# Kernel tuning notes

Measured on AMD Instinct MI355X. Metric: run time of the kernel, lower is better.

The kernel has to match this reference:

```python
import jax, jax.numpy as jnp
import numpy as np

B, C, H, W = 8, 192, 128, 128
NUM_HEADS = 4
EPS = 1e-12  # torch F.normalize default eps
DN = ('NCHW', 'OIHW', 'NCHW')


def setup_inputs() -> dict:
    key = jax.random.key(0)
    k1, k2, k3, k4 = jax.random.split(key, 4)
    x = jax.random.normal(k1, (B, C, H, W), dtype=jnp.float32)
    qkv_w = jax.random.normal(k2, (3 * C, C, 1, 1), dtype=jnp.float32) * 0.05
    dw_w = jax.random.normal(k3, (3 * C, 1, 3, 3), dtype=jnp.float32) * 0.1
    proj_w = jax.random.normal(k4, (C, C, 1, 1), dtype=jnp.float32) * 0.05
    temperature = jnp.ones((NUM_HEADS, 1, 1), dtype=jnp.float32)
    return {"x": x, "qkv_w": qkv_w, "dw_w": dw_w, "proj_w": proj_w,
            "temperature": temperature}


def _l2norm(t):
    # F.normalize(t, dim=-1): divide by max(||t||, eps)
    n = jnp.sqrt(jnp.sum(t * t, axis=-1, keepdims=True))
    return t / jnp.maximum(n, EPS)


def reference(x, qkv_w, dw_w, proj_w, temperature):
    b, c, h, w = x.shape
    nh = NUM_HEADS
    cph = c // nh
    # 1x1 conv -> depthwise 3x3 conv (groups = 3*dim)
    qkv = jax.lax.conv_general_dilated(x, qkv_w, (1, 1), 'VALID',
                                       dimension_numbers=DN)
    qkv = jax.lax.conv_general_dilated(qkv, dw_w, (1, 1), [(1, 1), (1, 1)],
                                       dimension_numbers=DN,
                                       feature_group_count=3 * c)
    q, k, v = jnp.split(qkv, 3, axis=1)
    # [b, nh, cph, h*w]
    q = q.reshape(b, nh, cph, h * w)
    k = k.reshape(b, nh, cph, h * w)
    v = v.reshape(b, nh, cph, h * w)
    q = _l2norm(q)
    k = _l2norm(k)
    # channel attention: [b, nh, cph, cph]
    attn = jnp.einsum('bhcn,bhdn->bhcd', q, k) * temperature
    attn = jax.nn.softmax(attn, axis=-1)
    out = jnp.einsum('bhcd,bhdn->bhcn', attn, v)
    out = out.reshape(b, c, h, w)
    return jax.lax.conv_general_dilated(out, proj_w, (1, 1), 'VALID',
                                        dimension_numbers=DN)
```

## Files before the change

### kernel.cpp

```cpp
#include <hip/hip_runtime.h>
#include <hip/hip_bf16.h>

typedef __hip_bfloat16 bf16;
typedef __attribute__((ext_vector_type(8))) __bf16 bf16x8;
typedef __attribute__((ext_vector_type(4))) float f32x4;

#define HW 16384

static __device__ __forceinline__ float b2f(bf16 v) { return __bfloat162float(v); }
static __device__ __forceinline__ bf16 f2b(float v) { return __float2bfloat16(v); }
static __device__ __forceinline__ float blo(unsigned int w) {
    return __uint_as_float(w << 16);
}
static __device__ __forceinline__ float bhi(unsigned int w) {
    return __uint_as_float(w & 0xffff0000u);
}
static __device__ __forceinline__ unsigned short f2bu(float v) {
    union { bf16 b; unsigned short u; } c; c.b = f2b(v); return c.u;
}
static __device__ __forceinline__ void stf(float* p, float v) { *p = v; }
static __device__ __forceinline__ void stf(bf16* p, float v)  { *p = f2b(v); }

static __device__ __forceinline__ void load8(const float* p, float* v) {
    const float4* q = (const float4*)p;
    float4 a = q[0], b = q[1];
    v[0] = a.x; v[1] = a.y; v[2] = a.z; v[3] = a.w;
    v[4] = b.x; v[5] = b.y; v[6] = b.z; v[7] = b.w;
}
static __device__ __forceinline__ void load8(const bf16* p, float* v) {
    uint4 u = *(const uint4*)p;
    v[0] = blo(u.x); v[1] = bhi(u.x); v[2] = blo(u.y); v[3] = bhi(u.y);
    v[4] = blo(u.z); v[5] = bhi(u.z); v[6] = blo(u.w); v[7] = bhi(u.w);
}

__global__ __launch_bounds__(256) void transpose_cast(
    const float* __restrict__ x, bf16* __restrict__ xT)
{
    __shared__ float T[64][65];
    const int k0 = blockIdx.x * 64, n0 = blockIdx.y * 64, b = blockIdx.z;
    const float* xb = x + ((size_t)(b * 192 + k0) << 14) + n0;

    for (int s = threadIdx.x; s < 64 * 16; s += 256) {
        int k = s >> 4, n4 = (s & 15) * 4;
        float4 v = *(const float4*)(xb + ((size_t)k << 14) + n4);
        T[k][n4] = v.x; T[k][n4 + 1] = v.y; T[k][n4 + 2] = v.z; T[k][n4 + 3] = v.w;
    }
    __syncthreads();

    bf16* xo = xT + ((size_t)b << 14) * 192 + (size_t)n0 * 192 + k0;
    for (int s = threadIdx.x; s < 64 * 8; s += 256) {
        int n = s >> 3, k8 = (s & 7) * 8;
        union { unsigned short u[8]; uint4 v; } o;
#pragma unroll
        for (int j = 0; j < 8; j++) o.u[j] = f2bu(T[k8 + j][n]);
        *(uint4*)(xo + (size_t)n * 192 + k8) = o.v;
    }
}

template <typename TY>
__global__ __launch_bounds__(256) void gemm_nk(
    const float* __restrict__ Wm, const bf16* __restrict__ Bt,
    TY* __restrict__ Y, int M, int N)
{
    const int mb = blockIdx.x, nb = blockIdx.y, b = blockIdx.z;
    const int m0 = mb * 64, n0 = nb * 128;
    TY* Yb = Y + (size_t)b * M * N;
    const bf16* Bb = Bt + ((size_t)b * N + n0) * 192;

    __shared__ __bf16 As[64][200];
    __shared__ __bf16 Bs[128][200];

    const int tid = threadIdx.x;
    for (int s = tid; s < 64 * 24; s += 256) {
        int m = s / 24, kq = (s % 24) * 8;
        float v[8];
        load8(Wm + (size_t)(m0 + m) * 192 + kq, v);
        bf16x8 pk;
#pragma unroll
        for (int j = 0; j < 8; j++) pk[j] = (__bf16)v[j];
        *(bf16x8*)&As[m][kq] = pk;
    }
    for (int s = tid; s < 128 * 24; s += 256) {
        int n = s / 24, kq = s % 24;
        *(uint4*)&Bs[n][kq * 8] = *(const uint4*)(Bb + (size_t)n * 192 + kq * 8);
    }
    __syncthreads();

    const int lane = tid & 63, wave = tid >> 6;
    const int wm = (wave & 1) * 32, wn = (wave >> 1) * 64;
    const int r16 = lane & 15, quad = lane >> 4;

    f32x4 acc[2][4];
#pragma unroll
    for (int i = 0; i < 2; i++)
#pragma unroll
        for (int f = 0; f < 4; f++) acc[i][f] = (f32x4){0.f, 0.f, 0.f, 0.f};

#pragma unroll
    for (int kc = 0; kc < 6; kc++) {
        const int kb = kc * 32 + quad * 8;
        bf16x8 a0 = *(const bf16x8*)&As[wm + r16][kb];
        bf16x8 a1 = *(const bf16x8*)&As[wm + 16 + r16][kb];
        bf16x8 b0 = *(const bf16x8*)&Bs[wn + r16][kb];
        bf16x8 b1 = *(const bf16x8*)&Bs[wn + 16 + r16][kb];
        bf16x8 b2 = *(const bf16x8*)&Bs[wn + 32 + r16][kb];
        bf16x8 b3 = *(const bf16x8*)&Bs[wn + 48 + r16][kb];
        acc[0][0] = __builtin_amdgcn_mfma_f32_16x16x32_bf16(a0, b0, acc[0][0], 0, 0, 0);
        acc[0][1] = __builtin_amdgcn_mfma_f32_16x16x32_bf16(a0, b1, acc[0][1], 0, 0, 0);
        acc[0][2] = __builtin_amdgcn_mfma_f32_16x16x32_bf16(a0, b2, acc[0][2], 0, 0, 0);
        acc[0][3] = __builtin_amdgcn_mfma_f32_16x16x32_bf16(a0, b3, acc[0][3], 0, 0, 0);
        acc[1][0] = __builtin_amdgcn_mfma_f32_16x16x32_bf16(a1, b0, acc[1][0], 0, 0, 0);
        acc[1][1] = __builtin_amdgcn_mfma_f32_16x16x32_bf16(a1, b1, acc[1][1], 0, 0, 0);
        acc[1][2] = __builtin_amdgcn_mfma_f32_16x16x32_bf16(a1, b2, acc[1][2], 0, 0, 0);
        acc[1][3] = __builtin_amdgcn_mfma_f32_16x16x32_bf16(a1, b3, acc[1][3], 0, 0, 0);
    }

#pragma unroll
    for (int i = 0; i < 2; i++)
#pragma unroll
        for (int f = 0; f < 4; f++) {
            int gr = m0 + wm + i * 16 + quad * 4;
            int gc = n0 + wn + f * 16 + r16;
#pragma unroll
            for (int r = 0; r < 4; r++)
                stf(Yb + (size_t)(gr + r) * N + gc, acc[i][f][r]);
        }
}

__global__ __launch_bounds__(256) void dwconv3x3(
    const bf16* __restrict__ in, const float* __restrict__ wdw,
    bf16* __restrict__ out)
{
    const int plane = blockIdx.x >> 2;
    const int ybase = (blockIdx.x & 3) << 5;
    const int c = plane % 576;
    const bf16* ip = in + ((size_t)plane << 14);

    __shared__ unsigned short Ls[34][128];

    for (int i = threadIdx.x; i < 34 * 16; i += 256) {
        int r = i >> 4, cx = i & 15;
        int y = ybase - 1 + r;
        uint4 v = make_uint4(0u, 0u, 0u, 0u);
        if (y >= 0 && y < 128) v = ((const uint4*)(ip + ((size_t)y << 7)))[cx];
        ((uint4*)Ls[r])[cx] = v;
    }

    float w[9];
#pragma unroll
    for (int i = 0; i < 9; i++) w[i] = wdw[c * 9 + i];

    __syncthreads();

    const int lr = threadIdx.x >> 3;
    const int c0 = (threadIdx.x & 7) << 4;

    float row[3][18];
#pragma unroll
    for (int r3 = 0; r3 < 3; r3++) {
        int rr = lr + r3;
        row[r3][0]  = c0 ? __uint_as_float((unsigned int)Ls[rr][c0 - 1] << 16) : 0.f;
        row[r3][17] = (c0 + 16 < 128) ? __uint_as_float((unsigned int)Ls[rr][c0 + 16] << 16) : 0.f;
        const uint4* rp = (const uint4*)&Ls[rr][c0];
        uint4 p0 = rp[0], p1 = rp[1];
        row[r3][1] = blo(p0.x); row[r3][2] = bhi(p0.x);
        row[r3][3] = blo(p0.y); row[r3][4] = bhi(p0.y);
        row[r3][5] = blo(p0.z); row[r3][6] = bhi(p0.z);
        row[r3][7] = blo(p0.w); row[r3][8] = bhi(p0.w);
        row[r3][9]  = blo(p1.x); row[r3][10] = bhi(p1.x);
        row[r3][11] = blo(p1.y); row[r3][12] = bhi(p1.y);
        row[r3][13] = blo(p1.z); row[r3][14] = bhi(p1.z);
        row[r3][15] = blo(p1.w); row[r3][16] = bhi(p1.w);
    }

    union { unsigned short s[16]; uint4 v[2]; } o;
#pragma unroll
    for (int j = 0; j < 16; j++) {
        float s = 0.f;
#pragma unroll
        for (int r3 = 0; r3 < 3; r3++)
            s += w[r3 * 3 + 0] * row[r3][j] + w[r3 * 3 + 1] * row[r3][j + 1]
               + w[r3 * 3 + 2] * row[r3][j + 2];
        o.s[j] = f2bu(s);
    }
    uint4* op = (uint4*)(out + ((size_t)plane << 14) + ((size_t)(ybase + lr) << 7) + c0);
    op[0] = o.v[0];
    op[1] = o.v[1];
}

__global__ __launch_bounds__(256) void rownorm(
    const bf16* __restrict__ qkv, float* __restrict__ rn)
{
    int r = blockIdx.x;
    int which = (r >= 1536) ? 1 : 0;
    int rr = r - which * 1536;
    int b = rr / 192, c = rr % 192;
    const bf16* p = qkv + ((size_t)(b * 576 + which * 192 + c) << 14);

    float s = 0.f;
    for (int i = threadIdx.x * 8; i < HW; i += 256 * 8) {
        float v[8];
        load8(p + i, v);
#pragma unroll
        for (int j = 0; j < 8; j++) s += v[j] * v[j];
    }
#pragma unroll
    for (int off = 32; off; off >>= 1) s += __shfl_down(s, off);
    __shared__ float red[4];
    if ((threadIdx.x & 63) == 0) red[threadIdx.x >> 6] = s;
    __syncthreads();
    if (threadIdx.x == 0) {
        float t = red[0] + red[1] + red[2] + red[3];
        rn[r] = 1.0f / fmaxf(sqrtf(t), 1e-12f);
    }
}

__global__ __launch_bounds__(256) void attn_dots(
    const bf16* __restrict__ qkv, float* __restrict__ attn)
{
    const int bh = blockIdx.y, b = bh >> 2, h = bh & 3;
    const int tid = threadIdx.x;
    const int wave = tid >> 6, lane = tid & 63;
    const int n0 = blockIdx.x * 1024 + wave * 256;
    const bf16* q  = qkv + ((size_t)(b * 576 + h * 48) << 14);
    const bf16* kp = qkv + ((size_t)(b * 576 + 192 + h * 48) << 14);

    __shared__ __bf16 S[4][2][48][72];

    const int r16 = lane & 15, quad = lane >> 4;

    f32x4 acc[3][3];
#pragma unroll
    for (int i = 0; i < 3; i++)
#pragma unroll
        for (int j = 0; j < 3; j++) acc[i][j] = (f32x4){0.f, 0.f, 0.f, 0.f};

    for (int t = 0; t < 4; t++) {
        const int nb = n0 + t * 64;
        for (int s = lane; s < 48 * 8; s += 64) {
            int c = s >> 3, seg = (s & 7) * 8;
            *(uint4*)&S[wave][0][c][seg] = *(const uint4*)(q  + ((size_t)c << 14) + nb + seg);
            *(uint4*)&S[wave][1][c][seg] = *(const uint4*)(kp + ((size_t)c << 14) + nb + seg);
        }
        __syncthreads();
#pragma unroll
        for (int half = 0; half < 2; half++) {
            const int kb = half * 32 + quad * 8;
            bf16x8 qa[3], ka[3];
#pragma unroll
            for (int i = 0; i < 3; i++) {
                qa[i] = *(const bf16x8*)&S[wave][0][i * 16 + r16][kb];
                ka[i] = *(const bf16x8*)&S[wave][1][i * 16 + r16][kb];
            }
#pragma unroll
            for (int i = 0; i < 3; i++)
#pragma unroll
                for (int j = 0; j < 3; j++)
                    acc[i][j] = __builtin_amdgcn_mfma_f32_16x16x32_bf16(
                        qa[i], ka[j], acc[i][j], 0, 0, 0);
        }
        __syncthreads();
    }

    float* ap = attn + (size_t)bh * 2304;
#pragma unroll
    for (int i = 0; i < 3; i++)
#pragma unroll
        for (int j = 0; j < 3; j++) {
            int c = i * 16 + quad * 4;
            int d = j * 16 + r16;
#pragma unroll
            for (int r = 0; r < 4; r++)
                atomicAdd(&ap[(c + r) * 48 + d], acc[i][j][r]);
        }
}

__global__ __launch_bounds__(64) void softmax48(
    float* __restrict__ attn, const float* __restrict__ rn,
    const float* __restrict__ temp)
{
    int bh = blockIdx.x, b = bh >> 2, h = bh & 3;
    int c = threadIdx.x;
    if (c >= 48) return;
    float t = temp[h];
    float iq = rn[b * 192 + h * 48 + c];
    const float* ik = rn + 1536 + b * 192 + h * 48;
    float* row = attn + (size_t)bh * 2304 + c * 48;

    float v[48];
    float mx = -1e30f;
#pragma unroll
    for (int d = 0; d < 48; d++) {
        v[d] = row[d] * iq * ik[d] * t;
        mx = fmaxf(mx, v[d]);
    }
    float s = 0.f;
#pragma unroll
    for (int d = 0; d < 48; d++) {
        v[d] = expf(v[d] - mx);
        s += v[d];
    }
    float inv = 1.0f / s;
#pragma unroll
    for (int d = 0; d < 48; d++) row[d] = v[d] * inv;
}

__global__ __launch_bounds__(256) void attn_v(
    const float* __restrict__ attn, const bf16* __restrict__ qkv,
    bf16* __restrict__ aout)
{
    int bh = blockIdx.y, b = bh >> 2, h = bh & 3;
    int n = blockIdx.x * 256 + threadIdx.x;

    __shared__ float A[48 * 48];
    for (int i = threadIdx.x; i < 2304; i += 256) A[i] = attn[(size_t)bh * 2304 + i];
    __syncthreads();

    const bf16* v = qkv + ((size_t)(b * 576 + 384 + h * 48) << 14) + n;
    float acc[48];
#pragma unroll
    for (int c = 0; c < 48; c++) acc[c] = 0.f;

    for (int d = 0; d < 48; d++) {
        float vd = b2f(v[(size_t)d << 14]);
#pragma unroll
        for (int c = 0; c < 48; c++) acc[c] += A[c * 48 + d] * vd;
    }
    union { unsigned short s[48]; uint4 v4[6]; } o;
#pragma unroll
    for (int c = 0; c < 48; c++) o.s[c] = f2bu(acc[c]);
    uint4* op = (uint4*)(aout + (((size_t)b << 14) + n) * 192 + h * 48);
#pragma unroll
    for (int j = 0; j < 6; j++) op[j] = o.v4[j];
}

extern "C" void kernel_launch(void* const* d_in, const int* in_sizes, int n_in,
                              void* d_out, int out_size, void* d_ws, size_t ws_size,
                              hipStream_t stream)
{
    const float* x      = (const float*)d_in[0];
    const float* qkv_w  = (const float*)d_in[1];
    const float* dw_w   = (const float*)d_in[2];
    const float* proj_w = (const float*)d_in[3];
    const float* temp   = (const float*)d_in[4];
    float* out = (float*)d_out;

    char* ws = (char*)d_ws;
    const size_t Q = (size_t)8 * 576 * HW * sizeof(bf16);
    bf16*  qkv0 = (bf16*)ws;
    bf16*  qkv1 = (bf16*)(ws + Q);
    bf16*  xT   = qkv1;
    float* attn = (float*)(ws + 2 * Q);
    float* rn   = (float*)(ws + 2 * Q + (size_t)32 * 2304 * sizeof(float));
    bf16*  aout = qkv0;

    transpose_cast<<<dim3(3, 256, 8), 256, 0, stream>>>(x, xT);
    gemm_nk<bf16><<<dim3(9, 128, 8), 256, 0, stream>>>(qkv_w, xT, qkv0, 576, HW);
    dwconv3x3<<<dim3(8 * 576 * 4), 256, 0, stream>>>(qkv0, dw_w, qkv1);
    rownorm<<<dim3(3072), 256, 0, stream>>>(qkv1, rn);
    hipMemsetAsync(attn, 0, (size_t)32 * 2304 * sizeof(float), stream);
    attn_dots<<<dim3(16, 32), 256, 0, stream>>>(qkv1, attn);
    softmax48<<<dim3(32), 64, 0, stream>>>(attn, rn, temp);
    attn_v<<<dim3(64, 32), 256, 0, stream>>>(attn, qkv1, aout);
    gemm_nk<float><<<dim3(3, 128, 8), 256, 0, stream>>>(proj_w, aout, out, 192, HW);
}
```

Before: 562.1 us.

## Fold attention into projection, fuse row norms into dwconv, drop transposes

The QKV GEMM now reads the fp32 NCHW input directly, packing bf16 pairs strided by HW, so the separate transpose/cast pass goes away. Squared row norms are accumulated with atomics inside the depthwise conv, which removes the rownorm pass. The attention matrix is premultiplied by the projection weights into a per-batch 192x192 matrix, so the final GEMM reads V directly and the attn_v pass with its intermediate buffer disappears. attn_dots now loads operands from global memory without LDS staging. The cost is uncoalesced strided B loads and A weights re-read from global and recast inside the GEMM loop.

After: 821.8 us. +46.2%, slower.

```diff
diff --git a/kernel.cpp b/kernel.cpp
--- a/kernel.cpp
+++ b/kernel.cpp
@@ -9,127 +9,81 @@
 
 static __device__ __forceinline__ float b2f(bf16 v) { return __bfloat162float(v); }
 static __device__ __forceinline__ bf16 f2b(float v) { return __float2bfloat16(v); }
-static __device__ __forceinline__ float blo(unsigned int w) {
-    return __uint_as_float(w << 16);
-}
-static __device__ __forceinline__ float bhi(unsigned int w) {
-    return __uint_as_float(w & 0xffff0000u);
-}
 static __device__ __forceinline__ unsigned short f2bu(float v) {
     union { bf16 b; unsigned short u; } c; c.b = f2b(v); return c.u;
 }
+static __device__ __forceinline__ float blo(unsigned int w) { return __uint_as_float(w << 16); }
+static __device__ __forceinline__ float bhi(unsigned int w) { return __uint_as_float(w & 0xffff0000u); }
+
+static __device__ __forceinline__ unsigned int loadpair(const float* p, int rs) {
+    return (unsigned int)f2bu(p[0]) | ((unsigned int)f2bu(p[rs]) << 16);
+}
+static __device__ __forceinline__ unsigned int loadpair(const bf16* p, int rs) {
+    union { bf16 b; unsigned short u; } a, c; a.b = p[0]; c.b = p[rs];
+    return (unsigned int)a.u | ((unsigned int)c.u << 16);
+}
 static __device__ __forceinline__ void stf(float* p, float v) { *p = v; }
-static __device__ __forceinline__ void stf(bf16* p, float v)  { *p = f2b(v); }
-
-static __device__ __forceinline__ void load8(const float* p, float* v) {
-    const float4* q = (const float4*)p;
-    float4 a = q[0], b = q[1];
-    v[0] = a.x; v[1] = a.y; v[2] = a.z; v[3] = a.w;
-    v[4] = b.x; v[5] = b.y; v[6] = b.z; v[7] = b.w;
-}
-static __device__ __forceinline__ void load8(const bf16* p, float* v) {
-    uint4 u = *(const uint4*)p;
-    v[0] = blo(u.x); v[1] = bhi(u.x); v[2] = blo(u.y); v[3] = bhi(u.y);
-    v[4] = blo(u.z); v[5] = bhi(u.z); v[6] = blo(u.w); v[7] = bhi(u.w);
-}
-
-__global__ __launch_bounds__(256) void transpose_cast(
-    const float* __restrict__ x, bf16* __restrict__ xT)
-{
-    __shared__ float T[64][65];
-    const int k0 = blockIdx.x * 64, n0 = blockIdx.y * 64, b = blockIdx.z;
-    const float* xb = x + ((size_t)(b * 192 + k0) << 14) + n0;
-
-    for (int s = threadIdx.x; s < 64 * 16; s += 256) {
-        int k = s >> 4, n4 = (s & 15) * 4;
-        float4 v = *(const float4*)(xb + ((size_t)k << 14) + n4);
-        T[k][n4] = v.x; T[k][n4 + 1] = v.y; T[k][n4 + 2] = v.z; T[k][n4 + 3] = v.w;
-    }
-    __syncthreads();
-
-    bf16* xo = xT + ((size_t)b << 14) * 192 + (size_t)n0 * 192 + k0;
-    for (int s = threadIdx.x; s < 64 * 8; s += 256) {
-        int n = s >> 3, k8 = (s & 7) * 8;
-        union { unsigned short u[8]; uint4 v; } o;
-#pragma unroll
-        for (int j = 0; j < 8; j++) o.u[j] = f2bu(T[k8 + j][n]);
-        *(uint4*)(xo + (size_t)n * 192 + k8) = o.v;
-    }
-}
-
-template <typename TY>
-__global__ __launch_bounds__(256) void gemm_nk(
-    const float* __restrict__ Wm, const bf16* __restrict__ Bt,
-    TY* __restrict__ Y, int M, int N)
-{
-    const int mb = blockIdx.x, nb = blockIdx.y, b = blockIdx.z;
-    const int m0 = mb * 64, n0 = nb * 128;
-    TY* Yb = Y + (size_t)b * M * N;
-    const bf16* Bb = Bt + ((size_t)b * N + n0) * 192;
-
-    __shared__ __bf16 As[64][200];
-    __shared__ __bf16 Bs[128][200];
-
-    const int tid = threadIdx.x;
-    for (int s = tid; s < 64 * 24; s += 256) {
-        int m = s / 24, kq = (s % 24) * 8;
-        float v[8];
-        load8(Wm + (size_t)(m0 + m) * 192 + kq, v);
-        bf16x8 pk;
-#pragma unroll
-        for (int j = 0; j < 8; j++) pk[j] = (__bf16)v[j];
-        *(bf16x8*)&As[m][kq] = pk;
-    }
-    for (int s = tid; s < 128 * 24; s += 256) {
-        int n = s / 24, kq = s % 24;
-        *(uint4*)&Bs[n][kq * 8] = *(const uint4*)(Bb + (size_t)n * 192 + kq * 8);
-    }
-    __syncthreads();
-
-    const int lane = tid & 63, wave = tid >> 6;
-    const int wm = (wave & 1) * 32, wn = (wave >> 1) * 64;
+static __device__ __forceinline__ void stf(bf16* p, float v) { *p = f2b(v); }
+
+template <typename TB, typename TY>
+__global__ __launch_bounds__(256) void gemm_fused(
+    const float* __restrict__ Wsrc, long wstride, int M,
+    const TB* __restrict__ Bsrc, long bstride,
+    TY* __restrict__ Y)
+{
+    const int n0 = blockIdx.x * 64, b = blockIdx.y;
+    const float* Wb = Wsrc + (size_t)b * wstride;
+    const TB* Bb = Bsrc + (size_t)b * bstride;
+    TY* Yb = Y + (size_t)b * M * HW;
+
+    const int lane = threadIdx.x & 63, wave = threadIdx.x >> 6;
     const int r16 = lane & 15, quad = lane >> 4;
-
-    f32x4 acc[2][4];
-#pragma unroll
-    for (int i = 0; i < 2; i++)
-#pragma unroll
-        for (int f = 0; f < 4; f++) acc[i][f] = (f32x4){0.f, 0.f, 0.f, 0.f};
-
+    const int n = n0 + wave * 16 + r16;
+
+    bf16x8 breg[6];
 #pragma unroll
     for (int kc = 0; kc < 6; kc++) {
-        const int kb = kc * 32 + quad * 8;
-        bf16x8 a0 = *(const bf16x8*)&As[wm + r16][kb];
-        bf16x8 a1 = *(const bf16x8*)&As[wm + 16 + r16][kb];
-        bf16x8 b0 = *(const bf16x8*)&Bs[wn + r16][kb];
-        bf16x8 b1 = *(const bf16x8*)&Bs[wn + 16 + r16][kb];
-        bf16x8 b2 = *(const bf16x8*)&Bs[wn + 32 + r16][kb];
-        bf16x8 b3 = *(const bf16x8*)&Bs[wn + 48 + r16][kb];
-        acc[0][0] = __builtin_amdgcn_mfma_f32_16x16x32_bf16(a0, b0, acc[0][0], 0, 0, 0);
-        acc[0][1] = __builtin_amdgcn_mfma_f32_16x16x32_bf16(a0, b1, acc[0][1], 0, 0, 0);
-        acc[0][2] = __builtin_amdgcn_mfma_f32_16x16x32_bf16(a0, b2, acc[0][2], 0, 0, 0);
-        acc[0][3] = __builtin_amdgcn_mfma_f32_16x16x32_bf16(a0, b3, acc[0][3], 0, 0, 0);
-        acc[1][0] = __builtin_amdgcn_mfma_f32_16x16x32_bf16(a1, b0, acc[1][0], 0, 0, 0);
-        acc[1][1] = __builtin_amdgcn_mfma_f32_16x16x32_bf16(a1, b1, acc[1][1], 0, 0, 0);
-        acc[1][2] = __builtin_amdgcn_mfma_f32_16x16x32_bf16(a1, b2, acc[1][2], 0, 0, 0);
-        acc[1][3] = __builtin_amdgcn_mfma_f32_16x16x32_bf16(a1, b3, acc[1][3], 0, 0, 0);
-    }
-
-#pragma unroll
-    for (int i = 0; i < 2; i++)
-#pragma unroll
-        for (int f = 0; f < 4; f++) {
-            int gr = m0 + wm + i * 16 + quad * 4;
-            int gc = n0 + wn + f * 16 + r16;
+        union { unsigned int u[4]; bf16x8 v; } pk;
+#pragma unroll
+        for (int i = 0; i < 4; i++) {
+            int k = kc * 32 + quad * 8 + 2 * i;
+            pk.u[i] = loadpair(Bb + ((size_t)k << 14) + n, HW);
+        }
+        breg[kc] = pk.v;
+    }
+
+    for (int m0 = 0; m0 < M; m0 += 64) {
+        f32x4 acc[4];
+#pragma unroll
+        for (int i = 0; i < 4; i++) acc[i] = (f32x4){0.f, 0.f, 0.f, 0.f};
+#pragma unroll
+        for (int kc = 0; kc < 6; kc++) {
+#pragma unroll
+            for (int i = 0; i < 4; i++) {
+                const float* ap = Wb + (size_t)(m0 + i * 16 + r16) * 192 + kc * 32 + quad * 8;
+                float4 x0 = *(const float4*)ap;
+                float4 x1 = *(const float4*)(ap + 4);
+                union { unsigned int u[4]; bf16x8 v; } af;
+                af.u[0] = (unsigned)f2bu(x0.x) | ((unsigned)f2bu(x0.y) << 16);
+                af.u[1] = (unsigned)f2bu(x0.z) | ((unsigned)f2bu(x0.w) << 16);
+                af.u[2] = (unsigned)f2bu(x1.x) | ((unsigned)f2bu(x1.y) << 16);
+                af.u[3] = (unsigned)f2bu(x1.z) | ((unsigned)f2bu(x1.w) << 16);
+                acc[i] = __builtin_amdgcn_mfma_f32_16x16x32_bf16(af.v, breg[kc], acc[i], 0, 0, 0);
+            }
+        }
+#pragma unroll
+        for (int i = 0; i < 4; i++) {
+            int gr = m0 + i * 16 + quad * 4;
 #pragma unroll
             for (int r = 0; r < 4; r++)
-                stf(Yb + (size_t)(gr + r) * N + gc, acc[i][f][r]);
-        }
+                stf(Yb + ((size_t)(gr + r) << 14) + n, acc[i][r]);
+        }
+    }
 }
 
 __global__ __launch_bounds__(256) void dwconv3x3(
     const bf16* __restrict__ in, const float* __restrict__ wdw,
-    bf16* __restrict__ out)
+    bf16* __restrict__ out, float* __restrict__ sq)
 {
     const int plane = blockIdx.x >> 2;
     const int ybase = (blockIdx.x & 3) << 5;
@@ -137,6 +91,7 @@
     const bf16* ip = in + ((size_t)plane << 14);
 
     __shared__ unsigned short Ls[34][128];
+    __shared__ float red[4];
 
     for (int i = threadIdx.x; i < 34 * 16; i += 256) {
         int r = i >> 4, cx = i & 15;
@@ -173,6 +128,7 @@
         row[r3][15] = blo(p1.w); row[r3][16] = bhi(p1.w);
     }
 
+    float ss = 0.f;
     union { unsigned short s[16]; uint4 v[2]; } o;
 #pragma unroll
     for (int j = 0; j < 16; j++) {
@@ -181,37 +137,23 @@
         for (int r3 = 0; r3 < 3; r3++)
             s += w[r3 * 3 + 0] * row[r3][j] + w[r3 * 3 + 1] * row[r3][j + 1]
                + w[r3 * 3 + 2] * row[r3][j + 2];
+        ss += s * s;
         o.s[j] = f2bu(s);
     }
     uint4* op = (uint4*)(out + ((size_t)plane << 14) + ((size_t)(ybase + lr) << 7) + c0);
     op[0] = o.v[0];
     op[1] = o.v[1];
-}
-
-__global__ __launch_bounds__(256) void rownorm(
-    const bf16* __restrict__ qkv, float* __restrict__ rn)
-{
-    int r = blockIdx.x;
-    int which = (r >= 1536) ? 1 : 0;
-    int rr = r - which * 1536;
-    int b = rr / 192, c = rr % 192;
-    const bf16* p = qkv + ((size_t)(b * 576 + which * 192 + c) << 14);
-
-    float s = 0.f;
-    for (int i = threadIdx.x * 8; i < HW; i += 256 * 8) {
-        float v[8];
-        load8(p + i, v);
-#pragma unroll
-        for (int j = 0; j < 8; j++) s += v[j] * v[j];
-    }
-#pragma unroll
-    for (int off = 32; off; off >>= 1) s += __shfl_down(s, off);
-    __shared__ float red[4];
-    if ((threadIdx.x & 63) == 0) red[threadIdx.x >> 6] = s;
-    __syncthreads();
-    if (threadIdx.x == 0) {
-        float t = red[0] + red[1] + red[2] + red[3];
-        rn[r] = 1.0f / fmaxf(sqrtf(t), 1e-12f);
+
+    if (c < 384) {
+#pragma unroll
+        for (int off = 32; off; off >>= 1) ss += __shfl_down(ss, off);
+        if ((threadIdx.x & 63) == 0) red[threadIdx.x >> 6] = ss;
+        __syncthreads();
+        if (threadIdx.x == 0) {
+            int b = plane / 576;
+            int rowi = (c < 192) ? (b * 192 + c) : (1536 + b * 192 + (c - 192));
+            atomicAdd(&sq[rowi], red[0] + red[1] + red[2] + red[3]);
+        }
     }
 }
 
@@ -219,15 +161,11 @@
     const bf16* __restrict__ qkv, float* __restrict__ attn)
 {
     const int bh = blockIdx.y, b = bh >> 2, h = bh & 3;
-    const int tid = threadIdx.x;
-    const int wave = tid >> 6, lane = tid & 63;
-    const int n0 = blockIdx.x * 1024 + wave * 256;
+    const int wave = threadIdx.x >> 6, lane = threadIdx.x & 63;
+    const int r16 = lane & 15, quad = lane >> 4;
     const bf16* q  = qkv + ((size_t)(b * 576 + h * 48) << 14);
     const bf16* kp = qkv + ((size_t)(b * 576 + 192 + h * 48) << 14);
-
-    __shared__ __bf16 S[4][2][48][72];
-
-    const int r16 = lane & 15, quad = lane >> 4;
+    const int nbase = (blockIdx.x * 4 + wave) * 512;
 
     f32x4 acc[3][3];
 #pragma unroll
@@ -235,31 +173,20 @@
 #pragma unroll
         for (int j = 0; j < 3; j++) acc[i][j] = (f32x4){0.f, 0.f, 0.f, 0.f};
 
-    for (int t = 0; t < 4; t++) {
-        const int nb = n0 + t * 64;
-        for (int s = lane; s < 48 * 8; s += 64) {
-            int c = s >> 3, seg = (s & 7) * 8;
-            *(uint4*)&S[wave][0][c][seg] = *(const uint4*)(q  + ((size_t)c << 14) + nb + seg);
-            *(uint4*)&S[wave][1][c][seg] = *(const uint4*)(kp + ((size_t)c << 14) + nb + seg);
-        }
-        __syncthreads();
-#pragma unroll
-        for (int half = 0; half < 2; half++) {
-            const int kb = half * 32 + quad * 8;
-            bf16x8 qa[3], ka[3];
-#pragma unroll
-            for (int i = 0; i < 3; i++) {
-                qa[i] = *(const bf16x8*)&S[wave][0][i * 16 + r16][kb];
-                ka[i] = *(const bf16x8*)&S[wave][1][i * 16 + r16][kb];
-            }
-#pragma unroll
-            for (int i = 0; i < 3; i++)
-#pragma unroll
-                for (int j = 0; j < 3; j++)
-                    acc[i][j] = __builtin_amdgcn_mfma_f32_16x16x32_bf16(
-                        qa[i], ka[j], acc[i][j], 0, 0, 0);
-        }
-        __syncthreads();
+    for (int t = 0; t < 16; t++) {
+        const int nb = nbase + t * 32 + quad * 8;
+        bf16x8 qa[3], ka[3];
+#pragma unroll
+        for (int i = 0; i < 3; i++) {
+            qa[i] = *(const bf16x8*)(q  + ((size_t)(i * 16 + r16) << 14) + nb);
+            ka[i] = *(const bf16x8*)(kp + ((size_t)(i * 16 + r16) << 14) + nb);
+        }
+#pragma unroll
+        for (int i = 0; i < 3; i++)
+#pragma unroll
+            for (int j = 0; j < 3; j++)
+                acc[i][j] = __builtin_amdgcn_mfma_f32_16x16x32_bf16(
+                    qa[i], ka[j], acc[i][j], 0, 0, 0);
     }
 
     float* ap = attn + (size_t)bh * 2304;
@@ -276,15 +203,17 @@
 }
 
 __global__ __launch_bounds__(64) void softmax48(
-    float* __restrict__ attn, const float* __restrict__ rn,
+    float* __restrict__ attn, const float* __restrict__ sq,
     const float* __restrict__ temp)
 {
     int bh = blockIdx.x, b = bh >> 2, h = bh & 3;
     int c = threadIdx.x;
+    __shared__ float ik[48];
+    if (c < 48) ik[c] = 1.0f / fmaxf(sqrtf(sq[1536 + b * 192 + h * 48 + c]), 1e-12f);
+    __syncthreads();
     if (c >= 48) return;
     float t = temp[h];
-    float iq = rn[b * 192 + h * 48 + c];
-    const float* ik = rn + 1536 + b * 192 + h * 48;
+    float iq = 1.0f / fmaxf(sqrtf(sq[b * 192 + h * 48 + c]), 1e-12f);
     float* row = attn + (size_t)bh * 2304 + c * 48;
 
     float v[48];
@@ -305,33 +234,32 @@
     for (int d = 0; d < 48; d++) row[d] = v[d] * inv;
 }
 
-__global__ __launch_bounds__(256) void attn_v(
-    const float* __restrict__ attn, const bf16* __restrict__ qkv,
-    bf16* __restrict__ aout)
-{
-    int bh = blockIdx.y, b = bh >> 2, h = bh & 3;
-    int n = blockIdx.x * 256 + threadIdx.x;
-
-    __shared__ float A[48 * 48];
-    for (int i = threadIdx.x; i < 2304; i += 256) A[i] = attn[(size_t)bh * 2304 + i];
+__global__ __launch_bounds__(256) void pmat(
+    const float* __restrict__ proj_w, const float* __restrict__ attn,
+    float* __restrict__ P)
+{
+    const int bh = blockIdx.x, b = bh >> 2, h = bh & 3;
+    __shared__ float A[48][49];
+    for (int i = threadIdx.x; i < 2304; i += 256)
+        A[i / 48][i % 48] = attn[(size_t)bh * 2304 + i];
     __syncthreads();
-
-    const bf16* v = qkv + ((size_t)(b * 576 + 384 + h * 48) << 14) + n;
-    float acc[48];
-#pragma unroll
-    for (int c = 0; c < 48; c++) acc[c] = 0.f;
-
+    const int m = threadIdx.x;
+    if (m >= 192) return;
+    float w[48];
+    const float4* pw = (const float4*)(proj_w + m * 192 + h * 48);
+#pragma unroll
+    for (int i = 0; i < 12; i++) {
+        float4 v = pw[i];
+        w[i * 4] = v.x; w[i * 4 + 1] = v.y; w[i * 4 + 2] = v.z; w[i * 4 + 3] = v.w;
+    }
+    float* Pr = P + (size_t)(b * 192 + m) * 192 + h * 48;
+#pragma unroll 4
     for (int d = 0; d < 48; d++) {
-        float vd = b2f(v[(size_t)d << 14]);
-#pragma unroll
-        for (int c = 0; c < 48; c++) acc[c] += A[c * 48 + d] * vd;
-    }
-    union { unsigned short s[48]; uint4 v4[6]; } o;
-#pragma unroll
-    for (int c = 0; c < 48; c++) o.s[c] = f2bu(acc[c]);
-    uint4* op = (uint4*)(aout + (((size_t)b << 14) + n) * 192 + h * 48);
-#pragma unroll
-    for (int j = 0; j < 6; j++) op[j] = o.v4[j];
+        float s = 0.f;
+#pragma unroll
+        for (int cc = 0; cc < 48; cc++) s += w[cc] * A[cc][d];
+        Pr[d] = s;
+    }
 }
 
 extern "C" void kernel_launch(void* const* d_in, const int* in_sizes, int n_in,
@@ -349,18 +277,17 @@
     const size_t Q = (size_t)8 * 576 * HW * sizeof(bf16);
     bf16*  qkv0 = (bf16*)ws;
     bf16*  qkv1 = (bf16*)(ws + Q);
-    bf16*  xT   = qkv1;
     float* attn = (float*)(ws + 2 * Q);
-    float* rn   = (float*)(ws + 2 * Q + (size_t)32 * 2304 * sizeof(float));
-    bf16*  aout = qkv0;
-
-    transpose_cast<<<dim3(3, 256, 8), 256, 0, stream>>>(x, xT);
-    gemm_nk<bf16><<<dim3(9, 128, 8), 256, 0, stream>>>(qkv_w, xT, qkv0, 576, HW);
-    dwconv3x3<<<dim3(8 * 576 * 4), 256, 0, stream>>>(qkv0, dw_w, qkv1);
-    rownorm<<<dim3(3072), 256, 0, stream>>>(qkv1, rn);
-    hipMemsetAsync(attn, 0, (size_t)32 * 2304 * sizeof(float), stream);
-    attn_dots<<<dim3(16, 32), 256, 0, stream>>>(qkv1, attn);
-    softmax48<<<dim3(32), 64, 0, stream>>>(attn, rn, temp);
-    attn_v<<<dim3(64, 32), 256, 0, stream>>>(attn, qkv1, aout);
-    gemm_nk<float><<<dim3(3, 128, 8), 256, 0, stream>>>(proj_w, aout, out, 192, HW);
-}
+    float* sq   = (float*)(ws + 2 * Q + 294912);
+    float* P    = (float*)ws;
+
+    hipMemsetAsync(attn, 0, 294912 + 12288, stream);
+    gemm_fused<float, bf16><<<dim3(256, 8), 256, 0, stream>>>(
+        qkv_w, 0L, 576, x, (long)192 * HW, qkv0);
+    dwconv3x3<<<dim3(8 * 576 * 4), 256, 0, stream>>>(qkv0, dw_w, qkv1, sq);
+    attn_dots<<<dim3(8, 32), 256, 0, stream>>>(qkv1, attn);
+    softmax48<<<dim3(32), 64, 0, stream>>>(attn, sq, temp);
+    pmat<<<dim3(32), 256, 0, stream>>>(proj_w, attn, P);
+    gemm_fused<bf16, float><<<dim3(256, 8), 256, 0, stream>>>(
+        P, (long)192 * 192, 192, qkv1 + (size_t)384 * HW, (long)576 * HW, out);
+}
```
